# Optimization experiments

Measured on AMD Instinct MI355X. Metric: run time of the kernel, lower is better.

## Reference

```python
import jax, jax.numpy as jnp
import numpy as np

N_CLASSES = 16
GAMMA = 2.0
MULT_UNLABELED = 3.0
EPS = 1e-6
B, C, D, H, W, K = 2, 16, 64, 128, 128, 4


def setup_inputs() -> dict:
    key = jax.random.key(0)
    k1, k2, k3 = jax.random.split(key, 3)
    # probs are softmax outputs over the class axis (axis=1)
    probs = jax.nn.softmax(jax.random.normal(k1, (B, C, D, H, W), dtype=jnp.float32), axis=1)
    target = jax.random.randint(k2, (B, D, H, W), 0, N_CLASSES, dtype=jnp.int32)
    annotated_fg_categories = jax.random.randint(k3, (B, K), 0, N_CLASSES, dtype=jnp.int32)
    return {"probs": probs, "target": target, "annotated_fg_categories": annotated_fg_categories}


def reference(probs, target, annotated_fg_categories):
    # ---- regularization: -mean_spatial( sum_c p * log(clamp(p)) ) per sample ----
    logp = jnp.log(jnp.clip(probs, EPS, 1.0 - EPS))
    ent = jnp.mean(jnp.sum(probs * logp, axis=1), axis=(1, 2, 3))  # [B]
    all_bg = jnp.all(target == 0, axis=(1, 2, 3))                  # sample fully unlabeled?
    mult = jnp.where(all_bg, MULT_UNLABELED, 1.0)
    batch = target.shape[0]
    reg = -jnp.sum(mult * ent) / batch

    # ---- balanced focal CE ----
    # Every voxel belongs to exactly one unique label of its patch, so the
    # per-unique-label concat + mean in the torch loop equals a per-voxel mean.
    classes = jnp.arange(N_CLASSES)
    ann = annotated_fg_categories
    annotated = jnp.any((ann[:, :, None] == classes[None, None, :]) & (ann[:, :, None] > 0), axis=1)  # [B,C]
    unannot = (~annotated).astype(probs.dtype)  # includes class 0 (never annotated as fg)
    # background voxels: p = sum of probs over unannotated categories
    s0 = jnp.einsum('bcdhw,bc->bdhw', probs, unannot)
    # foreground voxels: p = probs at the target class
    p_fg = jnp.take_along_axis(probs, target[:, None].astype(jnp.int32), axis=1)[:, 0]
    p = jnp.where(target > 0, p_fg, s0)  # [B,D,H,W]
    # focal term uses unclamped p; log is clamped (matches torch code)
    ce_vox = -jnp.power(1.0 - p, GAMMA) * jnp.log(jnp.clip(p, EPS, 1.0 - EPS))
    ce = jnp.mean(ce_vox)  # mean over voxels == mean of per-sample means (equal voxel counts)
    return (ce, reg)
```

## Files before the change

kernel.cpp:

```cpp
#include <hip/hip_runtime.h>
#include <math.h>

#define SPATIAL (64 * 128 * 128)
#define NCLS 16
#define NB 2
#define NBLK 2048
#define TPB 256

__global__ __launch_bounds__(TPB) void bce_main(
    const float* __restrict__ probs,
    const int*   __restrict__ target,
    const int*   __restrict__ ann,
    float*       __restrict__ partials)
{
    unsigned um[NB];
#pragma unroll
    for (int b = 0; b < NB; ++b) {
        unsigned a = 0;
#pragma unroll
        for (int k = 0; k < 4; ++k) {
            int c = ann[b * 4 + k];
            if (c > 0) a |= (1u << c);
        }
        um[b] = ~a & 0xFFFFu;
    }

    const int j = blockIdx.x * TPB + threadIdx.x;
    const int v = j * 4;
    const int b = v >> 20;
    const int s = v & (SPATIAL - 1);

    const int4 t4 = *reinterpret_cast<const int4*>(target + v);
    const int t[4] = {t4.x, t4.y, t4.z, t4.w};

    const float* pb = probs + (size_t)b * NCLS * SPATIAL + s;
    const unsigned m = um[b];

    float ent[4] = {0.f, 0.f, 0.f, 0.f};
    float s0[4]  = {0.f, 0.f, 0.f, 0.f};
    float pt[4]  = {0.f, 0.f, 0.f, 0.f};

#pragma unroll
    for (int c = 0; c < NCLS; ++c) {
        const float4 p4 = *reinterpret_cast<const float4*>(pb + (size_t)c * SPATIAL);
        const float p[4] = {p4.x, p4.y, p4.z, p4.w};
        const bool un = (m >> c) & 1u;
#pragma unroll
        for (int q = 0; q < 4; ++q) {
            const float pc = fminf(fmaxf(p[q], 1e-6f), 0.999999f);
            ent[q] = fmaf(p[q], __log2f(pc), ent[q]);
            if (un) s0[q] += p[q];
            if (c == t[q]) pt[q] = p[q];
        }
    }

    float ce_sum = 0.f;
    float ent_b  = 0.f;
    float cnt_b  = 0.f;
#pragma unroll
    for (int q = 0; q < 4; ++q) {
        const float p  = (t[q] > 0) ? pt[q] : s0[q];
        const float pc = fminf(fmaxf(p, 1e-6f), 0.999999f);
        const float om = 1.f - p;
        ce_sum += om * om * __log2f(pc);
        ent_b  += ent[q];
        cnt_b  += (t[q] != 0) ? 1.f : 0.f;
    }

    float vals[5];
    vals[0] = ce_sum;
    vals[1] = (b == 0) ? ent_b : 0.f;
    vals[2] = (b == 1) ? ent_b : 0.f;
    vals[3] = (b == 0) ? cnt_b : 0.f;
    vals[4] = (b == 1) ? cnt_b : 0.f;

    __shared__ float red[5][TPB / 64];
    const int lane = threadIdx.x & 63;
    const int wave = threadIdx.x >> 6;
#pragma unroll
    for (int qq = 0; qq < 5; ++qq) {
        float x = vals[qq];
#pragma unroll
        for (int off = 32; off > 0; off >>= 1)
            x += __shfl_down(x, off, 64);
        if (lane == 0) red[qq][wave] = x;
    }
    __syncthreads();
    if (threadIdx.x == 0) {
#pragma unroll
        for (int qq = 0; qq < 5; ++qq) {
            float x = 0.f;
#pragma unroll
            for (int w = 0; w < TPB / 64; ++w) x += red[qq][w];
            partials[qq * NBLK + blockIdx.x] = x;
        }
    }
}

__global__ __launch_bounds__(TPB) void bce_final(
    const float* __restrict__ partials, float* __restrict__ out)
{
    __shared__ float red[5][TPB / 64];
    float acc[5] = {0.f, 0.f, 0.f, 0.f, 0.f};
    for (int i = threadIdx.x; i < NBLK; i += TPB) {
#pragma unroll
        for (int qq = 0; qq < 5; ++qq) acc[qq] += partials[qq * NBLK + i];
    }
    const int lane = threadIdx.x & 63;
    const int wave = threadIdx.x >> 6;
#pragma unroll
    for (int qq = 0; qq < 5; ++qq) {
        float x = acc[qq];
#pragma unroll
        for (int off = 32; off > 0; off >>= 1)
            x += __shfl_down(x, off, 64);
        if (lane == 0) red[qq][wave] = x;
    }
    __syncthreads();
    if (threadIdx.x == 0) {
        float ce = 0.f, e0 = 0.f, e1 = 0.f, c0 = 0.f, c1 = 0.f;
#pragma unroll
        for (int w = 0; w < TPB / 64; ++w) {
            ce += red[0][w]; e0 += red[1][w]; e1 += red[2][w];
            c0 += red[3][w]; c1 += red[4][w];
        }
        const float LN2  = 0.69314718055994530942f;
        const float invS = 1.f / (float)SPATIAL;
        const float ent0 = e0 * LN2 * invS;
        const float ent1 = e1 * LN2 * invS;
        const float m0   = (c0 == 0.f) ? 3.f : 1.f;
        const float m1   = (c1 == 0.f) ? 3.f : 1.f;
        const float reg  = -(m0 * ent0 + m1 * ent1) * 0.5f;
        const float cef  = -(ce * LN2) / (float)(NB * SPATIAL);
        out[0] = cef;
        out[1] = reg;
    }
}

extern "C" void kernel_launch(void* const* d_in, const int* in_sizes, int n_in,
                              void* d_out, int out_size, void* d_ws, size_t ws_size,
                              hipStream_t stream) {
    const float* probs  = (const float*)d_in[0];
    const int*   target = (const int*)d_in[1];
    const int*   ann    = (const int*)d_in[2];
    float*       out    = (float*)d_out;
    float*       partials = (float*)d_ws;

    bce_main<<<NBLK, TPB, 0, stream>>>(probs, target, ann, partials);
    bce_final<<<1, TPB, 0, stream>>>(partials, out);
}
```

Measured before the change: 40.46 us.

## Fuse final reduction into main kernel via last-block atomic counter and hoist loads

Merges the two-kernel reduction into one kernel: each block publishes its partials, bumps an atomic counter, and the last block to arrive does the final reduction and writes the outputs. All 16 class loads are also issued up front, before the annotation mask is computed, to raise memory-level parallelism. This removes one kernel launch and its gap but adds a memset launch to reset the counter, plus fences and atomics in every block.

```diff
diff --git a/kernel.cpp b/kernel.cpp
--- a/kernel.cpp
+++ b/kernel.cpp
@@ -7,43 +7,42 @@
 #define NBLK 2048
 #define TPB 256
 
-__global__ __launch_bounds__(TPB) void bce_main(
+__global__ __launch_bounds__(TPB) void bce_fused(
     const float* __restrict__ probs,
     const int*   __restrict__ target,
     const int*   __restrict__ ann,
-    float*       __restrict__ partials)
+    float*       __restrict__ partials,
+    unsigned*    __restrict__ counter,
+    float*       __restrict__ out)
 {
-    unsigned um[NB];
-#pragma unroll
-    for (int b = 0; b < NB; ++b) {
-        unsigned a = 0;
-#pragma unroll
-        for (int k = 0; k < 4; ++k) {
-            int c = ann[b * 4 + k];
-            if (c > 0) a |= (1u << c);
-        }
-        um[b] = ~a & 0xFFFFu;
-    }
-
     const int j = blockIdx.x * TPB + threadIdx.x;
     const int v = j * 4;
     const int b = v >> 20;
     const int s = v & (SPATIAL - 1);
 
     const int4 t4 = *reinterpret_cast<const int4*>(target + v);
+    const float* pb = probs + (size_t)b * NCLS * SPATIAL + s;
+    float4 p4[NCLS];
+#pragma unroll
+    for (int c = 0; c < NCLS; ++c)
+        p4[c] = *reinterpret_cast<const float4*>(pb + (size_t)c * SPATIAL);
+
+    unsigned a = 0;
+#pragma unroll
+    for (int k = 0; k < 4; ++k) {
+        const int c = ann[b * 4 + k];
+        if (c > 0) a |= (1u << c);
+    }
+    const unsigned m = ~a & 0xFFFFu;
+
     const int t[4] = {t4.x, t4.y, t4.z, t4.w};
-
-    const float* pb = probs + (size_t)b * NCLS * SPATIAL + s;
-    const unsigned m = um[b];
-
     float ent[4] = {0.f, 0.f, 0.f, 0.f};
     float s0[4]  = {0.f, 0.f, 0.f, 0.f};
     float pt[4]  = {0.f, 0.f, 0.f, 0.f};
 
 #pragma unroll
     for (int c = 0; c < NCLS; ++c) {
-        const float4 p4 = *reinterpret_cast<const float4*>(pb + (size_t)c * SPATIAL);
-        const float p[4] = {p4.x, p4.y, p4.z, p4.w};
+        const float p[4] = {p4[c].x, p4[c].y, p4[c].z, p4[c].w};
         const bool un = (m >> c) & 1u;
 #pragma unroll
         for (int q = 0; q < 4; ++q) {
@@ -54,9 +53,7 @@
         }
     }
 
-    float ce_sum = 0.f;
-    float ent_b  = 0.f;
-    float cnt_b  = 0.f;
+    float ce_sum = 0.f, ent_b = 0.f, cnt_b = 0.f;
 #pragma unroll
     for (int q = 0; q < 4; ++q) {
         const float p  = (t[q] > 0) ? pt[q] : s0[q];
@@ -75,6 +72,7 @@
     vals[4] = (b == 1) ? cnt_b : 0.f;
 
     __shared__ float red[5][TPB / 64];
+    __shared__ int   lastFlag;
     const int lane = threadIdx.x & 63;
     const int wave = threadIdx.x >> 6;
 #pragma unroll
@@ -92,22 +90,25 @@
             float x = 0.f;
 #pragma unroll
             for (int w = 0; w < TPB / 64; ++w) x += red[qq][w];
-            partials[qq * NBLK + blockIdx.x] = x;
+            __hip_atomic_store(&partials[qq * NBLK + blockIdx.x], x,
+                               __ATOMIC_RELAXED, __HIP_MEMORY_SCOPE_AGENT);
         }
+        __threadfence();
+        const unsigned old = atomicAdd(counter, 1u);
+        lastFlag = (old == NBLK - 1) ? 1 : 0;
     }
-}
+    __syncthreads();
+    if (!lastFlag) return;
 
-__global__ __launch_bounds__(TPB) void bce_final(
-    const float* __restrict__ partials, float* __restrict__ out)
-{
-    __shared__ float red[5][TPB / 64];
+    __threadfence();
     float acc[5] = {0.f, 0.f, 0.f, 0.f, 0.f};
     for (int i = threadIdx.x; i < NBLK; i += TPB) {
 #pragma unroll
-        for (int qq = 0; qq < 5; ++qq) acc[qq] += partials[qq * NBLK + i];
+        for (int qq = 0; qq < 5; ++qq)
+            acc[qq] += __hip_atomic_load(&partials[qq * NBLK + i],
+                                         __ATOMIC_RELAXED, __HIP_MEMORY_SCOPE_AGENT);
     }
-    const int lane = threadIdx.x & 63;
-    const int wave = threadIdx.x >> 6;
+    __syncthreads();
 #pragma unroll
     for (int qq = 0; qq < 5; ++qq) {
         float x = acc[qq];
@@ -130,10 +131,8 @@
         const float ent1 = e1 * LN2 * invS;
         const float m0   = (c0 == 0.f) ? 3.f : 1.f;
         const float m1   = (c1 == 0.f) ? 3.f : 1.f;
-        const float reg  = -(m0 * ent0 + m1 * ent1) * 0.5f;
-        const float cef  = -(ce * LN2) / (float)(NB * SPATIAL);
-        out[0] = cef;
-        out[1] = reg;
+        out[0] = -(ce * LN2) / (float)(NB * SPATIAL);
+        out[1] = -(m0 * ent0 + m1 * ent1) * 0.5f;
     }
 }
 
@@ -144,8 +143,10 @@
     const int*   target = (const int*)d_in[1];
     const int*   ann    = (const int*)d_in[2];
     float*       out    = (float*)d_out;
-    float*       partials = (float*)d_ws;
 
-    bce_main<<<NBLK, TPB, 0, stream>>>(probs, target, ann, partials);
-    bce_final<<<1, TPB, 0, stream>>>(partials, out);
+    float*    partials = (float*)d_ws;
+    unsigned* counter  = (unsigned*)((char*)d_ws + 5 * NBLK * sizeof(float));
+
+    hipMemsetAsync(counter, 0, sizeof(unsigned), stream);
+    bce_fused<<<NBLK, TPB, 0, stream>>>(probs, target, ann, partials, counter, out);
 }
```

Measured after the change: 101.3 us. 150% more time.
